# Kernel tuning notes

Measured on AMD Instinct MI355X. Metric: run time of the kernel, lower is better.

The kernel has to match this reference:

```python
import jax, jax.numpy as jnp
import numpy as np

K = 3          # kernel_size
DIL = 2        # dilation
PAD = 2        # padding = dilation*(K-1)/2 so output spatial == input spatial
RANKS = 3
EPS = 1e-6


def _unfold(h):
    """Replicate-pad then extract KxK dilated patches -> (b, c, K*K, H, W).
    Kernel-position ordering matches torch.nn.Unfold (row-major kh*K+kw)."""
    b, c, H, W = h.shape
    p = jnp.pad(h, ((0, 0), (0, 0), (PAD, PAD), (PAD, PAD)), mode='edge')
    patches = [p[:, :, i * DIL:i * DIL + H, j * DIL:j * DIL + W]
               for i in range(K) for j in range(K)]
    return jnp.stack(patches, axis=2)  # (b, c, K*K, H, W)


def setup_inputs() -> dict:
    key = jax.random.key(0)
    k1, k2, k3 = jax.random.split(key, 3)
    B, C, H, W = 4, 64, 128, 128
    x = jax.random.normal(k1, (B, C, H, W), dtype=jnp.float32)
    W_head = jax.random.normal(k2, (64, 64), dtype=jnp.float32) * 0.05  # (out_c, in_c)
    W_tail = jax.random.normal(k3, (64, 64), dtype=jnp.float32) * 0.05  # (in_c, out_c)
    return {"x": x, "W_head": W_head, "W_tail": W_tail}


def reference(x, W_head, W_tail):
    res = x
    # 1x1 head conv (no bias) + ReLU
    h = jax.nn.relu(jnp.einsum('oc,bchw->bohw', W_head, x))
    # im2col: (b, C, K*K, H, W)
    X = _unfold(h)
    # NMF-style init: broadcast means over kernel / channel dims to rank r
    U = jnp.repeat(X.mean(axis=2, keepdims=True), RANKS, axis=2)  # (b,c,r,h,w)
    V = jnp.repeat(X.mean(axis=1, keepdims=True), RANKS, axis=1)  # (b,r,k,h,w)
    # one Lee-Seung multiplicative update (stage_num=1)
    num = jnp.einsum('bcrhw,bckhw->brkhw', U, X)
    den = jnp.einsum('bcrhw,bckhw->brkhw', U,
                     jnp.einsum('bcrhw,brkhw->bckhw', U, V))
    V = V * (num / (den + EPS))
    num = jnp.einsum('bckhw,brkhw->bcrhw', X, V)
    den = jnp.einsum('bckhw,brkhw->bcrhw',
                     jnp.einsum('bcrhw,brkhw->bckhw', U, V), V)
    U = U * (num / (den + EPS))
    center = (K // 2) * K + K // 2  # = 4
    UV = jnp.einsum('bcrhw,brkhw->bckhw', U, V[:, :, center:center + 1])[:, :, 0]
    out = jnp.einsum('co,bohw->bchw', W_tail, UV) + res
    return out
```

## Files before the change

### kernel.cpp

```cpp
#include <hip/hip_runtime.h>

#define HWC 16384
#define WD  128
#define NC  64
#define EPSV 1e-6f

typedef __attribute__((ext_vector_type(8))) short bf16x8;
typedef __attribute__((ext_vector_type(4))) float f32x4;
typedef __attribute__((ext_vector_type(4))) unsigned int u32x4;

__device__ __forceinline__ unsigned short f2bf(float f) {
  unsigned u = __builtin_bit_cast(unsigned, f);
  u = (u + 0x7FFFu + ((u >> 16) & 1u)) >> 16;
  return (unsigned short)u;
}
__device__ __forceinline__ float bfLo(unsigned pk) { return __builtin_bit_cast(float, pk << 16); }
__device__ __forceinline__ float bfHi(unsigned pk) { return __builtin_bit_cast(float, pk & 0xFFFF0000u); }
__device__ __forceinline__ int swz(int row, int colbytes) {
  return ((row << 7) + colbytes) ^ ((row & 7) << 4);
}
__device__ __forceinline__ bf16x8 pack8(float4 a, float4 b) {
  bf16x8 r;
  r[0] = (short)f2bf(a.x); r[1] = (short)f2bf(a.y);
  r[2] = (short)f2bf(a.z); r[3] = (short)f2bf(a.w);
  r[4] = (short)f2bf(b.x); r[5] = (short)f2bf(b.y);
  r[6] = (short)f2bf(b.z); r[7] = (short)f2bf(b.w);
  return r;
}

__global__ __launch_bounds__(512, 4) void k_fused(const float* __restrict__ x,
                                                  const float* __restrict__ Wh,
                                                  const float* __restrict__ Wt,
                                                  float* __restrict__ out) {
  __shared__ __align__(16) char smem[53248];
  unsigned short* xt = (unsigned short*)smem;
  unsigned short* hl = (unsigned short*)(smem + 26624);
  float* red = (float*)smem;
  unsigned short* uvb = (unsigned short*)smem;

  const int t = threadIdx.x, lane = t & 63, wv = t >> 6;
  const int bid0 = blockIdx.x;
  const int bid = ((bid0 & 7) << 7) | (bid0 >> 3);
  const int seg = bid & 1, y = (bid >> 1) & 127, b = bid >> 8;
  const int w0 = seg << 6;
  const int c0 = wv << 3;
  const int l15 = lane & 15, kg = lane >> 4;
  const int mt = wv & 3;
  const int mrow = (mt << 4) + l15;

  int gy[3];
  gy[0] = y >= 2 ? y - 2 : 0;
  gy[1] = y;
  gy[2] = y <= 125 ? y + 2 : 127;

  const float* xb = x + (size_t)b * (NC * HWC);

  bf16x8 ha0, ha1;
  {
    const float* wr = Wh + mrow * 64 + kg * 8;
    ha0 = pack8(*(const float4*)wr, *(const float4*)(wr + 4));
    ha1 = pack8(*(const float4*)(wr + 32), *(const float4*)(wr + 36));
  }

  {
    int colm = w0 - 2 + lane; if (colm < 0) colm = 0;
#pragma unroll
    for (int r = 0; r < 3; ++r) {
      const float* xr = xb + gy[r] * WD + colm;
      bf16x8 v;
#pragma unroll
      for (int u = 0; u < 8; ++u) v[u] = (short)f2bf(xr[(size_t)(c0 + u) * HWC]);
      *(bf16x8*)((char*)xt + swz(r * 68 + lane, c0 * 2)) = v;
    }
    if (lane < 12) {
      const int re = lane >> 2, e = lane & 3;
      int cole = w0 + 62 + e; if (cole > 127) cole = 127;
      const float* xr = xb + gy[re] * WD + cole;
      bf16x8 v;
#pragma unroll
      for (int u = 0; u < 8; ++u) v[u] = (short)f2bf(xr[(size_t)(c0 + u) * HWC]);
      *(bf16x8*)((char*)xt + swz(re * 68 + 64 + e, c0 * 2)) = v;
    }
  }
  __syncthreads();

  {
    const int ntBeg = (wv >> 2) ? 7 : 0;
    const int ntEnd = (wv >> 2) ? 13 : 7;
    const f32x4 z = {0.f, 0.f, 0.f, 0.f};
    for (int nt = ntBeg; nt < ntEnd; ++nt) {
      const int s = (nt << 4) + l15;
      const bf16x8 b0 = *(const bf16x8*)((char*)xt + swz(s, kg * 16));
      const bf16x8 b1 = *(const bf16x8*)((char*)xt + swz(s, 64 + kg * 16));
      f32x4 acc = __builtin_amdgcn_mfma_f32_16x16x32_bf16(ha0, b0, z, 0, 0, 0);
      acc = __builtin_amdgcn_mfma_f32_16x16x32_bf16(ha1, b1, acc, 0, 0, 0);
      const float v0 = acc[0] > 0.f ? acc[0] : 0.f;
      const float v1 = acc[1] > 0.f ? acc[1] : 0.f;
      const float v2 = acc[2] > 0.f ? acc[2] : 0.f;
      const float v3 = acc[3] > 0.f ? acc[3] : 0.f;
      uint2 pk2;
      pk2.x = (unsigned)f2bf(v0) | ((unsigned)f2bf(v1) << 16);
      pk2.y = (unsigned)f2bf(v2) | ((unsigned)f2bf(v3) << 16);
      *(uint2*)((char*)hl + swz(s, (mt * 16 + kg * 4) * 2)) = pk2;
    }
  }
  __syncthreads();

  const int pl = lane;
  u32x4 tap[9];
#pragma unroll
  for (int r = 0; r < 3; ++r)
#pragma unroll
    for (int kc = 0; kc < 3; ++kc)
      tap[r * 3 + kc] = *(const u32x4*)((char*)hl + swz(r * 68 + pl + 2 * kc, c0 * 2));

  float S = 0.f, sumk[9], A[9], mreg[8];
#pragma unroll
  for (int k = 0; k < 9; ++k) { sumk[k] = 0.f; A[k] = 0.f; }
#pragma unroll
  for (int c = 0; c < 8; ++c) {
    float tc[9];
#pragma unroll
    for (int k = 0; k < 9; ++k) {
      const unsigned w32 = tap[k][c >> 1];
      tc[k] = (c & 1) ? bfHi(w32) : bfLo(w32);
    }
    float m = 0.f;
#pragma unroll
    for (int k = 0; k < 9; ++k) m += tc[k];
    m *= (1.f / 9.f);
    mreg[c] = m;
    S += m * m;
#pragma unroll
    for (int k = 0; k < 9; ++k) { sumk[k] += tc[k]; A[k] += m * tc[k]; }
  }
  __syncthreads();

  {
    float2* cell = (float2*)&red[t * 22];
    cell[0] = make_float2(S, sumk[0]);
    cell[1] = make_float2(sumk[1], sumk[2]);
    cell[2] = make_float2(sumk[3], sumk[4]);
    cell[3] = make_float2(sumk[5], sumk[6]);
    cell[4] = make_float2(sumk[7], sumk[8]);
    cell[5] = make_float2(A[0], A[1]);
    cell[6] = make_float2(A[2], A[3]);
    cell[7] = make_float2(A[4], A[5]);
    cell[8] = make_float2(A[6], A[7]);
    red[t * 22 + 18] = A[8];
  }
  __syncthreads();

  for (int p = wv; p < 10; p += 8) {
    float2 f = {0.f, 0.f};
#pragma unroll
    for (int w2 = 0; w2 < 8; ++w2) {
      const float2 g = *(const float2*)&red[(w2 * 64 + lane) * 22 + 2 * p];
      f.x += g.x; f.y += g.y;
    }
    *(float2*)&red[lane * 22 + 2 * p] = f;
  }
  __syncthreads();

  float Vk[9], T = 0.f;
  {
    const float2* cell = (const float2*)&red[lane * 22];
    const float2 d0 = cell[0], d1 = cell[1], d2 = cell[2], d3 = cell[3], d4 = cell[4];
    const float2 d5 = cell[5], d6 = cell[6], d7 = cell[7], d8 = cell[8];
    const float a8 = red[lane * 22 + 18];
    const float Sf = d0.x;
    const float sk[9] = {d0.y, d1.x, d1.y, d2.x, d2.y, d3.x, d3.y, d4.x, d4.y};
    const float Ak[9] = {d5.x, d5.y, d6.x, d6.y, d7.x, d7.y, d8.x, d8.y, a8};
#pragma unroll
    for (int k = 0; k < 9; ++k) {
      const float nk = sk[k] * (1.f / 64.f);
      Vk[k] = nk * (Ak[k] / (3.f * nk * Sf + EPSV));
      T += Vk[k] * Vk[k];
    }
  }
  const float V4 = Vk[4];
  __syncthreads();

  bf16x8 ta0, ta1;
  {
    const float* wr = Wt + mrow * 64 + kg * 8;
    ta0 = pack8(*(const float4*)wr, *(const float4*)(wr + 4));
    ta1 = pack8(*(const float4*)(wr + 32), *(const float4*)(wr + 36));
  }

  {
    bf16x8 vv;
#pragma unroll
    for (int c = 0; c < 8; ++c) {
      float Bc = 0.f;
#pragma unroll
      for (int k = 0; k < 9; ++k) {
        const unsigned w32 = tap[k][c >> 1];
        const float tk = (c & 1) ? bfHi(w32) : bfLo(w32);
        Bc += tk * Vk[k];
      }
      const float m = mreg[c];
      const float Uc = m * (Bc / (3.f * m * T + EPSV));
      vv[c] = (short)f2bf(3.f * Uc * V4);
    }
    *(bf16x8*)((char*)uvb + swz(pl, c0 * 2)) = vv;
  }
  __syncthreads();

  const int n0 = (wv >> 2) << 1;
  const f32x4 z2 = {0.f, 0.f, 0.f, 0.f};
  const size_t gb = (size_t)b * (NC * HWC) + (size_t)y * WD + w0;
#pragma unroll
  for (int nt = n0; nt < n0 + 2; ++nt) {
    const int px = (nt << 4) + l15;
    const bf16x8 b0 = *(const bf16x8*)((char*)uvb + swz(px, kg * 16));
    const bf16x8 b1 = *(const bf16x8*)((char*)uvb + swz(px, 64 + kg * 16));
    f32x4 acc = __builtin_amdgcn_mfma_f32_16x16x32_bf16(ta0, b0, z2, 0, 0, 0);
    acc = __builtin_amdgcn_mfma_f32_16x16x32_bf16(ta1, b1, acc, 0, 0, 0);
#pragma unroll
    for (int j = 0; j < 4; ++j) {
      const int c2 = (mt << 4) + kg * 4 + j;
      const size_t off = gb + (size_t)c2 * HWC + px;
      out[off] = acc[j] + x[off];
    }
  }
}

extern "C" void kernel_launch(void* const* d_in, const int* in_sizes, int n_in,
                              void* d_out, int out_size, void* d_ws, size_t ws_size,
                              hipStream_t stream) {
  const float* x  = (const float*)d_in[0];
  const float* Wh = (const float*)d_in[1];
  const float* Wt = (const float*)d_in[2];
  float* out = (float*)d_out;

  k_fused<<<1024, 512, 0, stream>>>(x, Wh, Wt, out);
}
```

Measured before the change: 27.12 us.

## Remap pixel/channel work to lanes, shuffle-reduce channel sums, prefetch residual

Changes the post-head mapping so each wave handles 8 pixels with 8 lanes each covering 8 channels, instead of one pixel per lane across all waves. The cross-channel reduction then uses three xor-shuffle steps within the wave, replacing the LDS scratch reduction and its three block barriers. The residual x values are loaded into registers at kernel start so their latency overlaps the head stage. The head MFMA loop is also fully unrolled per wave half. The cost is more registers for the residual prefetch and for 57 shuffles per thread, which may lower occupancy.

```diff
diff --git a/kernel.cpp b/kernel.cpp
--- a/kernel.cpp
+++ b/kernel.cpp
@@ -35,7 +35,6 @@
   __shared__ __align__(16) char smem[53248];
   unsigned short* xt = (unsigned short*)smem;
   unsigned short* hl = (unsigned short*)(smem + 26624);
-  float* red = (float*)smem;
   unsigned short* uvb = (unsigned short*)smem;
 
   const int t = threadIdx.x, lane = t & 63, wv = t >> 6;
@@ -47,6 +46,7 @@
   const int l15 = lane & 15, kg = lane >> 4;
   const int mt = wv & 3;
   const int mrow = (mt << 4) + l15;
+  const int n0 = (wv >> 2) << 1;
 
   int gy[3];
   gy[0] = y >= 2 ? y - 2 : 0;
@@ -54,12 +54,24 @@
   gy[2] = y <= 125 ? y + 2 : 127;
 
   const float* xb = x + (size_t)b * (NC * HWC);
+  const size_t gb = (size_t)b * (NC * HWC) + (size_t)y * WD + w0;
 
   bf16x8 ha0, ha1;
   {
     const float* wr = Wh + mrow * 64 + kg * 8;
     ha0 = pack8(*(const float4*)wr, *(const float4*)(wr + 4));
     ha1 = pack8(*(const float4*)(wr + 32), *(const float4*)(wr + 36));
+  }
+
+  float resv[2][4];
+#pragma unroll
+  for (int q = 0; q < 2; ++q) {
+    const int px = ((n0 + q) << 4) + l15;
+#pragma unroll
+    for (int j = 0; j < 4; ++j) {
+      const int c2 = (mt << 4) + kg * 4 + j;
+      resv[q][j] = x[gb + (size_t)c2 * HWC + px];
+    }
   }
 
   {
@@ -84,35 +96,43 @@
   }
   __syncthreads();
 
-  {
-    const int ntBeg = (wv >> 2) ? 7 : 0;
-    const int ntEnd = (wv >> 2) ? 13 : 7;
-    const f32x4 z = {0.f, 0.f, 0.f, 0.f};
-    for (int nt = ntBeg; nt < ntEnd; ++nt) {
-      const int s = (nt << 4) + l15;
-      const bf16x8 b0 = *(const bf16x8*)((char*)xt + swz(s, kg * 16));
-      const bf16x8 b1 = *(const bf16x8*)((char*)xt + swz(s, 64 + kg * 16));
-      f32x4 acc = __builtin_amdgcn_mfma_f32_16x16x32_bf16(ha0, b0, z, 0, 0, 0);
-      acc = __builtin_amdgcn_mfma_f32_16x16x32_bf16(ha1, b1, acc, 0, 0, 0);
-      const float v0 = acc[0] > 0.f ? acc[0] : 0.f;
-      const float v1 = acc[1] > 0.f ? acc[1] : 0.f;
-      const float v2 = acc[2] > 0.f ? acc[2] : 0.f;
-      const float v3 = acc[3] > 0.f ? acc[3] : 0.f;
-      uint2 pk2;
-      pk2.x = (unsigned)f2bf(v0) | ((unsigned)f2bf(v1) << 16);
-      pk2.y = (unsigned)f2bf(v2) | ((unsigned)f2bf(v3) << 16);
-      *(uint2*)((char*)hl + swz(s, (mt * 16 + kg * 4) * 2)) = pk2;
-    }
-  }
+#define HEAD_STEP(NT)                                                            \
+  {                                                                              \
+    const int s = ((NT) << 4) + l15;                                             \
+    const bf16x8 b0 = *(const bf16x8*)((char*)xt + swz(s, kg * 16));             \
+    const bf16x8 b1 = *(const bf16x8*)((char*)xt + swz(s, 64 + kg * 16));        \
+    f32x4 acc = __builtin_amdgcn_mfma_f32_16x16x32_bf16(ha0, b0, zz, 0, 0, 0);   \
+    acc = __builtin_amdgcn_mfma_f32_16x16x32_bf16(ha1, b1, acc, 0, 0, 0);        \
+    const float v0 = acc[0] > 0.f ? acc[0] : 0.f;                                \
+    const float v1 = acc[1] > 0.f ? acc[1] : 0.f;                                \
+    const float v2 = acc[2] > 0.f ? acc[2] : 0.f;                                \
+    const float v3 = acc[3] > 0.f ? acc[3] : 0.f;                                \
+    uint2 pk2;                                                                   \
+    pk2.x = (unsigned)f2bf(v0) | ((unsigned)f2bf(v1) << 16);                     \
+    pk2.y = (unsigned)f2bf(v2) | ((unsigned)f2bf(v3) << 16);                     \
+    *(uint2*)((char*)hl + swz(s, (mt * 16 + kg * 4) * 2)) = pk2;                 \
+  }
+  {
+    const f32x4 zz = {0.f, 0.f, 0.f, 0.f};
+    if (wv < 4) {
+#pragma unroll
+      for (int nt = 0; nt < 7; ++nt) HEAD_STEP(nt)
+    } else {
+#pragma unroll
+      for (int nt = 7; nt < 13; ++nt) HEAD_STEP(nt)
+    }
+  }
+#undef HEAD_STEP
   __syncthreads();
 
-  const int pl = lane;
+  const int pxn = (wv << 3) | (lane >> 3);
+  const int cb2 = (lane & 7) << 4;
   u32x4 tap[9];
 #pragma unroll
   for (int r = 0; r < 3; ++r)
 #pragma unroll
     for (int kc = 0; kc < 3; ++kc)
-      tap[r * 3 + kc] = *(const u32x4*)((char*)hl + swz(r * 68 + pl + 2 * kc, c0 * 2));
+      tap[r * 3 + kc] = *(const u32x4*)((char*)hl + swz(r * 68 + pxn + 2 * kc, cb2));
 
   float S = 0.f, sumk[9], A[9], mreg[8];
 #pragma unroll
@@ -134,52 +154,24 @@
 #pragma unroll
     for (int k = 0; k < 9; ++k) { sumk[k] += tc[k]; A[k] += m * tc[k]; }
   }
-  __syncthreads();
-
-  {
-    float2* cell = (float2*)&red[t * 22];
-    cell[0] = make_float2(S, sumk[0]);
-    cell[1] = make_float2(sumk[1], sumk[2]);
-    cell[2] = make_float2(sumk[3], sumk[4]);
-    cell[3] = make_float2(sumk[5], sumk[6]);
-    cell[4] = make_float2(sumk[7], sumk[8]);
-    cell[5] = make_float2(A[0], A[1]);
-    cell[6] = make_float2(A[2], A[3]);
-    cell[7] = make_float2(A[4], A[5]);
-    cell[8] = make_float2(A[6], A[7]);
-    red[t * 22 + 18] = A[8];
-  }
-  __syncthreads();
-
-  for (int p = wv; p < 10; p += 8) {
-    float2 f = {0.f, 0.f};
-#pragma unroll
-    for (int w2 = 0; w2 < 8; ++w2) {
-      const float2 g = *(const float2*)&red[(w2 * 64 + lane) * 22 + 2 * p];
-      f.x += g.x; f.y += g.y;
-    }
-    *(float2*)&red[lane * 22 + 2 * p] = f;
-  }
-  __syncthreads();
+
+#pragma unroll
+  for (int d = 1; d <= 4; d <<= 1) {
+    S += __shfl_xor(S, d);
+#pragma unroll
+    for (int k = 0; k < 9; ++k) sumk[k] += __shfl_xor(sumk[k], d);
+#pragma unroll
+    for (int k = 0; k < 9; ++k) A[k] += __shfl_xor(A[k], d);
+  }
 
   float Vk[9], T = 0.f;
-  {
-    const float2* cell = (const float2*)&red[lane * 22];
-    const float2 d0 = cell[0], d1 = cell[1], d2 = cell[2], d3 = cell[3], d4 = cell[4];
-    const float2 d5 = cell[5], d6 = cell[6], d7 = cell[7], d8 = cell[8];
-    const float a8 = red[lane * 22 + 18];
-    const float Sf = d0.x;
-    const float sk[9] = {d0.y, d1.x, d1.y, d2.x, d2.y, d3.x, d3.y, d4.x, d4.y};
-    const float Ak[9] = {d5.x, d5.y, d6.x, d6.y, d7.x, d7.y, d8.x, d8.y, a8};
-#pragma unroll
-    for (int k = 0; k < 9; ++k) {
-      const float nk = sk[k] * (1.f / 64.f);
-      Vk[k] = nk * (Ak[k] / (3.f * nk * Sf + EPSV));
-      T += Vk[k] * Vk[k];
-    }
+#pragma unroll
+  for (int k = 0; k < 9; ++k) {
+    const float nk = sumk[k] * (1.f / 64.f);
+    Vk[k] = nk * (A[k] / (3.f * nk * S + EPSV));
+    T += Vk[k] * Vk[k];
   }
   const float V4 = Vk[4];
-  __syncthreads();
 
   bf16x8 ta0, ta1;
   {
@@ -203,16 +195,14 @@
       const float Uc = m * (Bc / (3.f * m * T + EPSV));
       vv[c] = (short)f2bf(3.f * Uc * V4);
     }
-    *(bf16x8*)((char*)uvb + swz(pl, c0 * 2)) = vv;
+    *(bf16x8*)((char*)uvb + swz(pxn, cb2)) = vv;
   }
   __syncthreads();
 
-  const int n0 = (wv >> 2) << 1;
   const f32x4 z2 = {0.f, 0.f, 0.f, 0.f};
-  const size_t gb = (size_t)b * (NC * HWC) + (size_t)y * WD + w0;
-#pragma unroll
-  for (int nt = n0; nt < n0 + 2; ++nt) {
-    const int px = (nt << 4) + l15;
+#pragma unroll
+  for (int q = 0; q < 2; ++q) {
+    const int px = ((n0 + q) << 4) + l15;
     const bf16x8 b0 = *(const bf16x8*)((char*)uvb + swz(px, kg * 16));
     const bf16x8 b1 = *(const bf16x8*)((char*)uvb + swz(px, 64 + kg * 16));
     f32x4 acc = __builtin_amdgcn_mfma_f32_16x16x32_bf16(ta0, b0, z2, 0, 0, 0);
@@ -221,7 +211,7 @@
     for (int j = 0; j < 4; ++j) {
       const int c2 = (mt << 4) + kg * 4 + j;
       const size_t off = gb + (size_t)c2 * HWC + px;
-      out[off] = acc[j] + x[off];
+      out[off] = acc[j] + resv[q][j];
     }
   }
 }
```

Result: slower. 37.46 us (+38.1%).
